# Kernel optimization log

Hardware: AMD Instinct MI355X
Metric: run time of the kernel (lower is better)

## Reference

```python
import jax, jax.numpy as jnp
import numpy as np

B, N, D = 8, 2048, 512


def setup_inputs() -> dict:
    key = jax.random.key(0)
    ks = jax.random.split(key, 16)
    s = 1.0 / np.sqrt(D)  # ~ torch Linear default init scale
    inp = {
        "X": jax.random.normal(ks[0], (B, N, D), jnp.float32),
        "Y": jax.random.normal(ks[1], (B, N, D), jnp.float32),
    }
    names = ["xq", "xk", "xv", "yq", "yk", "yv"]
    for i, nm in enumerate(names):
        inp[f"W_{nm}"] = jax.random.uniform(ks[2 + 2 * i], (D, D), jnp.float32, -s, s)
        inp[f"b_{nm}"] = jax.random.uniform(ks[3 + 2 * i], (D,), jnp.float32, -s, s)
    return inp


def _lin(x, W, b):
    # torch nn.Linear: x @ W^T + b
    return jnp.einsum("bnd,ed->bne", x, W) + b


def reference(X, Y, W_xq, b_xq, W_xk, b_xk, W_xv, b_xv, W_yq, b_yq, W_yk, b_yk, W_yv, b_yv):
    d = X.shape[-1]
    scale = 1.0 / jnp.sqrt(jnp.asarray(d, X.dtype))
    Q1, K1, V1 = _lin(X, W_xq, b_xq), _lin(X, W_xk, b_xk), _lin(X, W_xv, b_xv)
    Q2, K2, V2 = _lin(Y, W_yq, b_yq), _lin(Y, W_yk, b_yk), _lin(Y, W_yv, b_yv)
    # NOTE: F.softmax called without dim on a 3-D tensor -> torch legacy dim=0 (batch axis).
    S1 = jnp.einsum("bnd,bmd->bnm", Q1, K2) * scale  # [B, N, N]
    A1 = jax.nn.softmax(S1, axis=0)
    U_A1 = X + jnp.einsum("bnm,bmd->bnd", A1, V2)  # dropout = identity (eval)
    S2 = jnp.einsum("bnd,bmd->bnm", Q2, K1) * scale
    A2 = jax.nn.softmax(S2, axis=0)
    U_A2 = Y + jnp.einsum("bnm,bmd->bnd", A2, V1)
    return U_A1 + U_A2
```

## Files before the change

kernel.cpp:

```cpp
#include <hip/hip_runtime.h>

typedef unsigned short u16;
typedef __attribute__((ext_vector_type(8))) short bf16x8;
typedef __attribute__((ext_vector_type(4))) float f32x4;
typedef __attribute__((ext_vector_type(8))) u16 u16x8;

#define GLOAD_LDS(g, s) __builtin_amdgcn_global_load_lds( \
    (const __attribute__((address_space(1))) void*)(g),   \
    (__attribute__((address_space(3))) void*)(s), 16, 0, 0)

__device__ __forceinline__ u16 f2bf(float f) {
  union { float f; unsigned u; } v; v.f = f;
  unsigned r = v.u + 0x7fffu + ((v.u >> 16) & 1u);
  return (u16)(r >> 16);
}
__device__ __forceinline__ float bf2f(u16 h) {
  union { unsigned u; float f; } v; v.u = ((unsigned)h) << 16;
  return v.f;
}

__device__ __forceinline__ unsigned lds_a(const u16* p) {
  return (unsigned)(unsigned long long)(__attribute__((address_space(3))) const u16*)p;
}
__device__ __forceinline__ bf16x8 ds128(const u16* p) {
  bf16x8 r;
  asm volatile("ds_read_b128 %0, %1" : "=v"(r) : "v"(lds_a(p)));
  return r;
}

__device__ __forceinline__ void stage_pair(const u16* gA, int lda, const u16* gB, int ldb,
                                           u16* lA, u16* lB, int wave, int lane) {
  int row = (wave << 4) + (lane >> 2);
  int kb  = (lane & 3) << 3;
  GLOAD_LDS(gA + row * lda + kb,        lA + (wave << 9));
  GLOAD_LDS(gA + (row + 64) * lda + kb, lA + ((wave + 4) << 9));
  GLOAD_LDS(gB + row * ldb + kb,        lB + (wave << 9));
  GLOAD_LDS(gB + (row + 64) * ldb + kb, lB + ((wave + 4) << 9));
}

__device__ __forceinline__ void gemm_seg(f32x4 (&acc)[4][4],
    const u16* Ag, const u16* Bg, int lda, int ldb, int nk,
    u16* As, u16* Bs, int wave, int lane) {
  const int wr = (wave >> 1) << 6, wc = (wave & 1) << 6;
  const int rl = lane & 15, rk = (lane >> 4) << 3;
  stage_pair(Ag, lda, Bg, ldb, As, Bs, wave, lane);
  if (nk > 1)
    stage_pair(Ag + 32, lda, Bg + 32, ldb, As + 4096, Bs + 4096, wave, lane);
  int bufsel = 0;
  for (int kt = 0; kt < nk; ++kt) {
    if (kt + 1 < nk) asm volatile("s_waitcnt vmcnt(4)" ::: "memory");
    else             asm volatile("s_waitcnt vmcnt(0)" ::: "memory");
    __builtin_amdgcn_s_barrier();
    asm volatile("" ::: "memory");
    if (kt + 2 < nk) {
      int nb = bufsel + 2; if (nb >= 3) nb -= 3;
      stage_pair(Ag + (long)(kt + 2) * 32, lda, Bg + (long)(kt + 2) * 32, ldb,
                 As + nb * 4096, Bs + nb * 4096, wave, lane);
    }
    const u16* ab = As + bufsel * 4096;
    const u16* bb = Bs + bufsel * 4096;
    bf16x8 af[4], bfr[4];
#pragma unroll
    for (int i = 0; i < 4; i++)
      af[i]  = *(const bf16x8*)(ab + ((wr + (i << 4) + rl) << 5) + rk);
#pragma unroll
    for (int j = 0; j < 4; j++)
      bfr[j] = *(const bf16x8*)(bb + ((wc + (j << 4) + rl) << 5) + rk);
#pragma unroll
    for (int i = 0; i < 4; i++)
#pragma unroll
      for (int j = 0; j < 4; j++)
        acc[i][j] = __builtin_amdgcn_mfma_f32_16x16x32_bf16(af[i], bfr[j], acc[i][j], 0, 0, 0);
    __builtin_amdgcn_sched_barrier(0);
    bufsel = bufsel + 1; if (bufsel == 3) bufsel = 0;
  }
}


__device__ __forceinline__ void stage256(const u16* gA, int lda, const u16* gB, int ldb,
                                         u16* Ad, u16* Bd, int tid) {
  int rw = tid >> 3, g0 = tid & 7;
  int gs = (g0 ^ (rw & 7)) << 3;
  int wb = (tid >> 6) << 9;
#pragma unroll
  for (int h = 0; h < 2; h++)
#pragma unroll
    for (int r = 0; r < 2; r++) {
      int row = h * 128 + r * 64 + rw;
      GLOAD_LDS(gA + (long)row * lda + gs, Ad + h * 8192 + r * 4096 + wb);
    }
#pragma unroll
  for (int r = 0; r < 2; r++) {
    int row = r * 64 + rw;
    GLOAD_LDS(gB + (long)row * ldb + gs, Bd + r * 4096 + wb);
  }
}

__device__ __forceinline__ void gemm256(f32x4 (&acc)[4][4],
    const u16* Ag, int lda, const u16* Bg, int ldb, int nk,
    u16* As, u16* Bs, int tid) {
  const int lane = tid & 63, wid = tid >> 6;
  const int mq = wid >> 1, nh = wid & 1;
  const int rl = lane & 15, kg = lane >> 4;
  const int swz0 = ((kg ^ (rl & 7)) << 3);
  const int rbA = (mq >> 1) * 8192 + ((mq & 1) * 64 + rl) * 64;
  const int rbB = (nh * 64 + rl) * 64;

  stage256(Ag, lda, Bg, ldb, As, Bs, tid);
  if (nk > 1)
    stage256(Ag + 64, lda, Bg + 64, ldb, As + 16384, Bs + 8192, tid);
  int bsel = 0;
  for (int t = 0; t < nk; ++t) {
    if (t + 1 < nk) asm volatile("s_waitcnt vmcnt(6)" ::: "memory");
    else            asm volatile("s_waitcnt vmcnt(0)" ::: "memory");
    __builtin_amdgcn_s_barrier();
    if (t + 2 < nk) {
      int nb = bsel + 2; if (nb >= 3) nb -= 3;
      stage256(Ag + (long)(t + 2) * 64, lda, Bg + (long)(t + 2) * 64, ldb,
               As + nb * 16384, Bs + nb * 8192, tid);
    }
    const u16* ab = As + bsel * 16384 + rbA;
    const u16* bb = Bs + bsel * 8192 + rbB;
    const int s0 = swz0, s1 = swz0 ^ 32;
    bf16x8 a0[4], b0[4], a1[4], b1[4];
#pragma unroll
    for (int i = 0; i < 4; i++) a0[i] = ds128(ab + i * 1024 + s0);
#pragma unroll
    for (int j = 0; j < 4; j++) b0[j] = ds128(bb + j * 1024 + s0);
#pragma unroll
    for (int i = 0; i < 4; i++) a1[i] = ds128(ab + i * 1024 + s1);
#pragma unroll
    for (int j = 0; j < 4; j++) b1[j] = ds128(bb + j * 1024 + s1);
    asm volatile("s_waitcnt lgkmcnt(8)" ::: "memory");
    __builtin_amdgcn_sched_barrier(0);
    __builtin_amdgcn_s_setprio(1);
#pragma unroll
    for (int i = 0; i < 4; i++)
#pragma unroll
      for (int j = 0; j < 4; j++)
        acc[i][j] = __builtin_amdgcn_mfma_f32_16x16x32_bf16(a0[i], b0[j], acc[i][j], 0, 0, 0);
    __builtin_amdgcn_s_setprio(0);
    asm volatile("s_waitcnt lgkmcnt(0)" ::: "memory");
    __builtin_amdgcn_sched_barrier(0);
    __builtin_amdgcn_s_setprio(1);
#pragma unroll
    for (int i = 0; i < 4; i++)
#pragma unroll
      for (int j = 0; j < 4; j++)
        acc[i][j] = __builtin_amdgcn_mfma_f32_16x16x32_bf16(a1[i], b1[j], acc[i][j], 0, 0, 0);
    __builtin_amdgcn_s_setprio(0);
    __builtin_amdgcn_sched_barrier(0);
    bsel = bsel + 1; if (bsel == 3) bsel = 0;
  }
}

__global__ __launch_bounds__(256) void k_cvt2(const float* __restrict__ inX,
                                              const float* __restrict__ inY,
                                              u16* __restrict__ oX, u16* __restrict__ oY,
                                              int n8) {
  int i = blockIdx.x * 256 + threadIdx.x;
  const float* in = (i < n8) ? inX : inY;
  u16* out = (i < n8) ? oX : oY;
  int k = (i < n8) ? i : i - n8;
  const float4* pf = (const float4*)in + (long)k * 2;
  float4 a = pf[0], b = pf[1];
  u16x8 o;
  o[0] = f2bf(a.x); o[1] = f2bf(a.y); o[2] = f2bf(a.z); o[3] = f2bf(a.w);
  o[4] = f2bf(b.x); o[5] = f2bf(b.y); o[6] = f2bf(b.z); o[7] = f2bf(b.w);
  *((u16x8*)out + k) = o;
}

struct P6 { const float* p[6]; };
struct O6 { u16* p[6]; };

__global__ __launch_bounds__(256) void k_cvt_w(P6 w, u16* __restrict__ out) {
  int z = blockIdx.y;
  int i = blockIdx.x * 256 + threadIdx.x;
  const float4* pf = (const float4*)w.p[z] + (long)i * 2;
  float4 a = pf[0], b = pf[1];
  u16x8 o;
  o[0] = f2bf(a.x); o[1] = f2bf(a.y); o[2] = f2bf(a.z); o[3] = f2bf(a.w);
  o[4] = f2bf(b.x); o[5] = f2bf(b.y); o[6] = f2bf(b.z); o[7] = f2bf(b.w);
  *((u16x8*)(out + (long)z * 262144) + i) = o;
}

__global__ __launch_bounds__(256) void k_proj(const u16* __restrict__ Xb, const u16* __restrict__ Yb,
                                              const u16* __restrict__ Wb, P6 bias, O6 dst) {
  __shared__ u16 As[12288], Bs[12288];
  int x = blockIdx.x;
  int swz = (x & 7) * 384 + (x >> 3);
  int bm = swz / 24;
  int r  = swz - bm * 24;
  int z = r >> 2, bn = r & 3;
  int tid = threadIdx.x, wave = tid >> 6, lane = tid & 63;
  const u16* Ag = (z < 3 ? Xb : Yb) + (long)bm * 128 * 512;
  const u16* Bg = Wb + (long)z * 262144 + (long)bn * 128 * 512;
  f32x4 acc[4][4] = {};
  gemm_seg(acc, Ag, Bg, 512, 512, 16, As, Bs, wave, lane);
  const float* bi = bias.p[z];
  u16* D = dst.p[z];
  int wr = (wave >> 1) << 6, wc = (wave & 1) << 6;
  int row0 = bm * 128 + wr + ((lane >> 4) << 2);
  int col0 = bn * 128 + wc + (lane & 15);
  float bj[4];
#pragma unroll
  for (int j = 0; j < 4; j++) bj[j] = bi[col0 + (j << 4)];
#pragma unroll
  for (int i = 0; i < 4; i++)
#pragma unroll
    for (int j = 0; j < 4; j++)
#pragma unroll
      for (int rr = 0; rr < 4; rr++)
        D[(long)(row0 + (i << 4) + rr) * 512 + col0 + (j << 4)] = f2bf(acc[i][j][rr] + bj[j]);
}

__global__ __launch_bounds__(512) void k_s(const u16* __restrict__ Q, const u16* __restrict__ K,
                                           u16* __restrict__ S) {
  __shared__ u16 As[49152], Bs[24576];
  int x = blockIdx.x;
  int swz = (x & 7) * 128 + (x >> 3);
  int bn = swz & 15, bm = (swz >> 4) & 7, b = swz >> 7;
  int tid = threadIdx.x;
  const u16* Ag = Q + (long)b * 1048576 + (long)bm * 256 * 512;
  const u16* Bg = K + (long)b * 1048576 + (long)bn * 128 * 512;
  f32x4 acc[4][4] = {};
  gemm256(acc, Ag, 512, Bg, 512, 8, As, Bs, tid);
  u16* D = S + (long)b * 4194304;
  const float scale = 0.04419417382415922f;
  int lane = tid & 63, wid = tid >> 6;
  int mq = wid >> 1, nh = wid & 1;
  int row0 = bm * 256 + mq * 64 + ((lane >> 4) << 2);
  int col0 = bn * 128 + nh * 64 + (lane & 15);
#pragma unroll
  for (int i = 0; i < 4; i++)
#pragma unroll
    for (int j = 0; j < 4; j++)
#pragma unroll
      for (int rr = 0; rr < 4; rr++)
        D[(long)(row0 + (i << 4) + rr) * 2048 + col0 + (j << 4)] = f2bf(acc[i][j][rr] * scale);
}

__global__ __launch_bounds__(256) void k_softmax(u16* __restrict__ S) {
  int idx = blockIdx.x * 256 + threadIdx.x;
  u16x8 v[8];
#pragma unroll
  for (int b = 0; b < 8; b++) v[b] = *((const u16x8*)(S + (long)b * 4194304) + idx);
#pragma unroll
  for (int j = 0; j < 8; j++) {
    float e[8], m = -1e30f;
#pragma unroll
    for (int b = 0; b < 8; b++) { e[b] = bf2f(v[b][j]); m = fmaxf(m, e[b]); }
    float s = 0.f;
#pragma unroll
    for (int b = 0; b < 8; b++) { e[b] = __expf(e[b] - m); s += e[b]; }
    float inv = 1.0f / s;
#pragma unroll
    for (int b = 0; b < 8; b++) v[b][j] = f2bf(e[b] * inv);
  }
#pragma unroll
  for (int b = 0; b < 8; b++) *((u16x8*)(S + (long)b * 4194304) + idx) = v[b];
}

__global__ __launch_bounds__(256) void k_tr(const u16* __restrict__ V1, const u16* __restrict__ V2,
                                            u16* __restrict__ T1, u16* __restrict__ T2) {
  __shared__ u16 tile[64][65];
  int z = blockIdx.z;
  const u16* src = (z < 8 ? V1 : V2) + (long)(z & 7) * 1048576;
  u16*       dst = (z < 8 ? T1 : T2) + (long)(z & 7) * 1048576;
  int n0 = blockIdx.x * 64, d0 = blockIdx.y * 64;
  int t = threadIdx.x;
  int r = t >> 2, cs = (t & 3) * 16;
  const u16x8* sp = (const u16x8*)(src + (long)(n0 + r) * 512 + d0 + cs);
  u16x8 a = sp[0], b = sp[1];
#pragma unroll
  for (int jj = 0; jj < 8; jj++) { tile[r][cs + jj] = a[jj]; tile[r][cs + 8 + jj] = b[jj]; }
  __syncthreads();
  u16x8 o0, o1;
#pragma unroll
  for (int jj = 0; jj < 8; jj++) { o0[jj] = tile[cs + jj][r]; o1[jj] = tile[cs + 8 + jj][r]; }
  u16x8* op = (u16x8*)(dst + (long)(d0 + r) * 2048 + n0 + cs);
  op[0] = o0; op[1] = o1;
}

__global__ __launch_bounds__(512) void k_pv(const u16* __restrict__ A, const u16* __restrict__ Vt,
                                            const float* __restrict__ X, const float* __restrict__ Y,
                                            float* __restrict__ out, int mode) {
  __shared__ u16 As[49152], Bs[24576];
  int x = blockIdx.x;
  int swz = (x & 7) * 32 + (x >> 3);
  int bn = swz & 3, bm = (swz >> 2) & 7, b = swz >> 5;
  int tid = threadIdx.x;
  const u16* Ag = A + (long)b * 4194304 + (long)bm * 256 * 2048;
  const u16* Bg = Vt + (long)b * 1048576 + (long)bn * 128 * 2048;
  f32x4 acc[4][4] = {};
  gemm256(acc, Ag, 2048, Bg, 2048, 32, As, Bs, tid);
  int lane = tid & 63, wid = tid >> 6;
  int mq = wid >> 1, nh = wid & 1;
  int row0 = bm * 256 + mq * 64 + ((lane >> 4) << 2);
  int col0 = bn * 128 + nh * 64 + (lane & 15);
  long base = (long)b * 1048576;
#pragma unroll
  for (int i = 0; i < 4; i++)
#pragma unroll
    for (int j = 0; j < 4; j++)
#pragma unroll
      for (int rr = 0; rr < 4; rr++) {
        long idx = base + (long)(row0 + (i << 4) + rr) * 512 + col0 + (j << 4);
        float v = acc[i][j][rr];
        out[idx] = mode ? (out[idx] + v) : (v + X[idx] + Y[idx]);
      }
}

extern "C" void kernel_launch(void* const* d_in, const int* in_sizes, int n_in,
                              void* d_out, int out_size, void* d_ws, size_t ws_size,
                              hipStream_t stream) {
  const float* X = (const float*)d_in[0];
  const float* Y = (const float*)d_in[1];
  P6 wp, bp;
  for (int i = 0; i < 6; i++) { wp.p[i] = (const float*)d_in[2 + 2 * i]; bp.p[i] = (const float*)d_in[3 + 2 * i]; }

  const long NX = 8L * 2048 * 512;
  const long NS = 8L * 2048 * 2048;
  u16* p = (u16*)d_ws;
  u16* Xb = p;  p += NX;
  u16* Yb = p;  p += NX;
  u16* Wb = p;  p += 6L * 512 * 512;
  u16* Q1 = p;  p += NX;
  u16* K2 = p;  p += NX;
  u16* Q2 = p;  p += NX;
  u16* K1 = p;  p += NX;
  u16* Sb = p;  p += NS;
  u16* V1 = Sb;
  u16* V2 = Sb + NX;
  u16* Vt1 = Xb;
  u16* Vt2 = Yb;
  (void)ws_size; (void)in_sizes; (void)n_in; (void)out_size;

  dim3 T(256);
  k_cvt2<<<dim3(8192), T, 0, stream>>>(X, Y, Xb, Yb, (int)(NX / 8));
  k_cvt_w<<<dim3(128, 6), T, 0, stream>>>(wp, Wb);
  O6 dst; dst.p[0] = Q1; dst.p[1] = K1; dst.p[2] = V1; dst.p[3] = Q2; dst.p[4] = K2; dst.p[5] = V2;
  k_proj<<<dim3(3072), T, 0, stream>>>(Xb, Yb, Wb, bp, dst);
  k_tr<<<dim3(32, 8, 16), T, 0, stream>>>(V1, V2, Vt1, Vt2);
  k_s<<<dim3(1024), dim3(512), 0, stream>>>(Q2, K1, Sb);
  k_softmax<<<dim3(2048), T, 0, stream>>>(Sb);
  k_pv<<<dim3(256), dim3(512), 0, stream>>>(Sb, Vt1, X, Y, (float*)d_out, 0);
  k_s<<<dim3(1024), dim3(512), 0, stream>>>(Q1, K2, Sb);
  k_softmax<<<dim3(2048), T, 0, stream>>>(Sb);
  k_pv<<<dim3(256), dim3(512), 0, stream>>>(Sb, Vt2, X, Y, (float*)d_out, 1);
}
```

Baseline: 362.1 us.

## Replace 256x128 triple-buffered GEMM with 128x128 double-buffered tiles in S and PV

The S and PV GEMMs move from a 512-thread, 256x128 block tile with a three-stage LDS ring to a 256-thread, 128x128 tile with two LDS buffers and a barrier at the end of each k-step. This cuts LDS use per block and doubles the grid, aiming for better occupancy and load balance across CUs. In exchange, operand reuse per block drops and the pipeline becomes shallower, since every iteration now waits for all global loads before its barrier, which can expose memory latency.

```diff
diff --git a/kernel.cpp b/kernel.cpp
--- a/kernel.cpp
+++ b/kernel.cpp
@@ -77,60 +77,45 @@
 }
 
 
-__device__ __forceinline__ void stage256(const u16* gA, int lda, const u16* gB, int ldb,
+__device__ __forceinline__ void stage128(const u16* gA, int lda, const u16* gB, int ldb,
                                          u16* Ad, u16* Bd, int tid) {
-  int rw = tid >> 3, g0 = tid & 7;
-  int gs = (g0 ^ (rw & 7)) << 3;
+  int rw = tid >> 3;
+  int gs = ((tid & 7) ^ (rw & 7)) << 3;
   int wb = (tid >> 6) << 9;
 #pragma unroll
-  for (int h = 0; h < 2; h++)
-#pragma unroll
-    for (int r = 0; r < 2; r++) {
-      int row = h * 128 + r * 64 + rw;
-      GLOAD_LDS(gA + (long)row * lda + gs, Ad + h * 8192 + r * 4096 + wb);
-    }
-#pragma unroll
-  for (int r = 0; r < 2; r++) {
-    int row = r * 64 + rw;
-    GLOAD_LDS(gB + (long)row * ldb + gs, Bd + r * 4096 + wb);
+  for (int p = 0; p < 4; p++) {
+    GLOAD_LDS(gA + (long)(p * 32 + rw) * lda + gs, Ad + p * 2048 + wb);
+    GLOAD_LDS(gB + (long)(p * 32 + rw) * ldb + gs, Bd + p * 2048 + wb);
   }
 }
 
-__device__ __forceinline__ void gemm256(f32x4 (&acc)[4][4],
+__device__ __forceinline__ void gemm128(f32x4 (&acc)[4][4],
     const u16* Ag, int lda, const u16* Bg, int ldb, int nk,
     u16* As, u16* Bs, int tid) {
   const int lane = tid & 63, wid = tid >> 6;
-  const int mq = wid >> 1, nh = wid & 1;
+  const int wr = (wid >> 1) << 6, wc = (wid & 1) << 6;
   const int rl = lane & 15, kg = lane >> 4;
-  const int swz0 = ((kg ^ (rl & 7)) << 3);
-  const int rbA = (mq >> 1) * 8192 + ((mq & 1) * 64 + rl) * 64;
-  const int rbB = (nh * 64 + rl) * 64;
-
-  stage256(Ag, lda, Bg, ldb, As, Bs, tid);
-  if (nk > 1)
-    stage256(Ag + 64, lda, Bg + 64, ldb, As + 16384, Bs + 8192, tid);
-  int bsel = 0;
+  const int swz0 = (kg ^ (rl & 7)) << 3;
+  const int rbA = (wr + rl) * 64, rbB = (wc + rl) * 64;
+
+  stage128(Ag, lda, Bg, ldb, As, Bs, tid);
+  asm volatile("s_waitcnt vmcnt(0)" ::: "memory");
+  __builtin_amdgcn_s_barrier();
   for (int t = 0; t < nk; ++t) {
-    if (t + 1 < nk) asm volatile("s_waitcnt vmcnt(6)" ::: "memory");
-    else            asm volatile("s_waitcnt vmcnt(0)" ::: "memory");
-    __builtin_amdgcn_s_barrier();
-    if (t + 2 < nk) {
-      int nb = bsel + 2; if (nb >= 3) nb -= 3;
-      stage256(Ag + (long)(t + 2) * 64, lda, Bg + (long)(t + 2) * 64, ldb,
-               As + nb * 16384, Bs + nb * 8192, tid);
-    }
-    const u16* ab = As + bsel * 16384 + rbA;
-    const u16* bb = Bs + bsel * 8192 + rbB;
-    const int s0 = swz0, s1 = swz0 ^ 32;
+    if (t + 1 < nk)
+      stage128(Ag + (t + 1) * 64, lda, Bg + (t + 1) * 64, ldb,
+               As + ((t + 1) & 1) * 8192, Bs + ((t + 1) & 1) * 8192, tid);
+    const u16* ab = As + (t & 1) * 8192 + rbA;
+    const u16* bb = Bs + (t & 1) * 8192 + rbB;
     bf16x8 a0[4], b0[4], a1[4], b1[4];
 #pragma unroll
-    for (int i = 0; i < 4; i++) a0[i] = ds128(ab + i * 1024 + s0);
-#pragma unroll
-    for (int j = 0; j < 4; j++) b0[j] = ds128(bb + j * 1024 + s0);
-#pragma unroll
-    for (int i = 0; i < 4; i++) a1[i] = ds128(ab + i * 1024 + s1);
-#pragma unroll
-    for (int j = 0; j < 4; j++) b1[j] = ds128(bb + j * 1024 + s1);
+    for (int i = 0; i < 4; i++) a0[i] = ds128(ab + i * 1024 + swz0);
+#pragma unroll
+    for (int j = 0; j < 4; j++) b0[j] = ds128(bb + j * 1024 + swz0);
+#pragma unroll
+    for (int i = 0; i < 4; i++) a1[i] = ds128(ab + i * 1024 + (swz0 ^ 32));
+#pragma unroll
+    for (int j = 0; j < 4; j++) b1[j] = ds128(bb + j * 1024 + (swz0 ^ 32));
     asm volatile("s_waitcnt lgkmcnt(8)" ::: "memory");
     __builtin_amdgcn_sched_barrier(0);
     __builtin_amdgcn_s_setprio(1);
@@ -150,7 +135,8 @@
         acc[i][j] = __builtin_amdgcn_mfma_f32_16x16x32_bf16(a1[i], b1[j], acc[i][j], 0, 0, 0);
     __builtin_amdgcn_s_setprio(0);
     __builtin_amdgcn_sched_barrier(0);
-    bsel = bsel + 1; if (bsel == 3) bsel = 0;
+    if (t + 1 < nk) asm volatile("s_waitcnt vmcnt(0)" ::: "memory");
+    __builtin_amdgcn_s_barrier();
   }
 }
 
@@ -214,23 +200,23 @@
         D[(long)(row0 + (i << 4) + rr) * 512 + col0 + (j << 4)] = f2bf(acc[i][j][rr] + bj[j]);
 }
 
-__global__ __launch_bounds__(512) void k_s(const u16* __restrict__ Q, const u16* __restrict__ K,
+__global__ __launch_bounds__(256) void k_s(const u16* __restrict__ Q, const u16* __restrict__ K,
                                            u16* __restrict__ S) {
-  __shared__ u16 As[49152], Bs[24576];
+  __shared__ u16 As[16384], Bs[16384];
   int x = blockIdx.x;
-  int swz = (x & 7) * 128 + (x >> 3);
-  int bn = swz & 15, bm = (swz >> 4) & 7, b = swz >> 7;
+  int swz = (x & 7) * 256 + (x >> 3);
+  int bn = swz & 15, bm = (swz >> 4) & 15, b = swz >> 8;
   int tid = threadIdx.x;
-  const u16* Ag = Q + (long)b * 1048576 + (long)bm * 256 * 512;
+  const u16* Ag = Q + (long)b * 1048576 + (long)bm * 128 * 512;
   const u16* Bg = K + (long)b * 1048576 + (long)bn * 128 * 512;
   f32x4 acc[4][4] = {};
-  gemm256(acc, Ag, 512, Bg, 512, 8, As, Bs, tid);
+  gemm128(acc, Ag, 512, Bg, 512, 8, As, Bs, tid);
   u16* D = S + (long)b * 4194304;
   const float scale = 0.04419417382415922f;
   int lane = tid & 63, wid = tid >> 6;
-  int mq = wid >> 1, nh = wid & 1;
-  int row0 = bm * 256 + mq * 64 + ((lane >> 4) << 2);
-  int col0 = bn * 128 + nh * 64 + (lane & 15);
+  int wr = (wid >> 1) << 6, wc = (wid & 1) << 6;
+  int row0 = bm * 128 + wr + ((lane >> 4) << 2);
+  int col0 = bn * 128 + wc + (lane & 15);
 #pragma unroll
   for (int i = 0; i < 4; i++)
 #pragma unroll
@@ -282,22 +268,22 @@
   op[0] = o0; op[1] = o1;
 }
 
-__global__ __launch_bounds__(512) void k_pv(const u16* __restrict__ A, const u16* __restrict__ Vt,
+__global__ __launch_bounds__(256) void k_pv(const u16* __restrict__ A, const u16* __restrict__ Vt,
                                             const float* __restrict__ X, const float* __restrict__ Y,
                                             float* __restrict__ out, int mode) {
-  __shared__ u16 As[49152], Bs[24576];
+  __shared__ u16 As[16384], Bs[16384];
   int x = blockIdx.x;
-  int swz = (x & 7) * 32 + (x >> 3);
-  int bn = swz & 3, bm = (swz >> 2) & 7, b = swz >> 5;
+  int swz = (x & 7) * 64 + (x >> 3);
+  int bn = swz & 3, bm = (swz >> 2) & 15, b = swz >> 6;
   int tid = threadIdx.x;
-  const u16* Ag = A + (long)b * 4194304 + (long)bm * 256 * 2048;
+  const u16* Ag = A + (long)b * 4194304 + (long)bm * 128 * 2048;
   const u16* Bg = Vt + (long)b * 1048576 + (long)bn * 128 * 2048;
   f32x4 acc[4][4] = {};
-  gemm256(acc, Ag, 2048, Bg, 2048, 32, As, Bs, tid);
+  gemm128(acc, Ag, 2048, Bg, 2048, 32, As, Bs, tid);
   int lane = tid & 63, wid = tid >> 6;
-  int mq = wid >> 1, nh = wid & 1;
-  int row0 = bm * 256 + mq * 64 + ((lane >> 4) << 2);
-  int col0 = bn * 128 + nh * 64 + (lane & 15);
+  int wr = (wid >> 1) << 6, wc = (wid & 1) << 6;
+  int row0 = bm * 128 + wr + ((lane >> 4) << 2);
+  int col0 = bn * 128 + wc + (lane & 15);
   long base = (long)b * 1048576;
 #pragma unroll
   for (int i = 0; i < 4; i++)
@@ -342,10 +328,10 @@
   O6 dst; dst.p[0] = Q1; dst.p[1] = K1; dst.p[2] = V1; dst.p[3] = Q2; dst.p[4] = K2; dst.p[5] = V2;
   k_proj<<<dim3(3072), T, 0, stream>>>(Xb, Yb, Wb, bp, dst);
   k_tr<<<dim3(32, 8, 16), T, 0, stream>>>(V1, V2, Vt1, Vt2);
-  k_s<<<dim3(1024), dim3(512), 0, stream>>>(Q2, K1, Sb);
+  k_s<<<dim3(2048), T, 0, stream>>>(Q2, K1, Sb);
   k_softmax<<<dim3(2048), T, 0, stream>>>(Sb);
-  k_pv<<<dim3(256), dim3(512), 0, stream>>>(Sb, Vt1, X, Y, (float*)d_out, 0);
-  k_s<<<dim3(1024), dim3(512), 0, stream>>>(Q1, K2, Sb);
+  k_pv<<<dim3(512), T, 0, stream>>>(Sb, Vt1, X, Y, (float*)d_out, 0);
+  k_s<<<dim3(2048), T, 0, stream>>>(Q1, K2, Sb);
   k_softmax<<<dim3(2048), T, 0, stream>>>(Sb);
-  k_pv<<<dim3(256), dim3(512), 0, stream>>>(Sb, Vt2, X, Y, (float*)d_out, 1);
-}
+  k_pv<<<dim3(512), T, 0, stream>>>(Sb, Vt2, X, Y, (float*)d_out, 1);
+}
```

Measured after the change: 367.6 us. About the same (+1.5%).
